# Performance work log

Measured on AMD Instinct MI355X. Metric: run time of the kernel, lower is better.

Reference implementation:

```python
import jax, jax.numpy as jnp
import numpy as np

B, S, D, H = 1, 4096, 1024, 16
HD = D // H

def setup_inputs() -> dict:
    key = jax.random.key(0)
    ks = jax.random.split(key, 6)
    scale = 0.02
    return {
        "x":  jax.random.normal(ks[0], (B, S, D), dtype=jnp.float32),
        "Wq": jax.random.normal(ks[1], (D, D), dtype=jnp.float32) * scale,
        "Wk": jax.random.normal(ks[2], (D, D), dtype=jnp.float32) * scale,
        "Wv": jax.random.normal(ks[3], (D, D), dtype=jnp.float32) * scale,
        "Wo": jax.random.normal(ks[4], (D, D), dtype=jnp.float32) * scale,
        "bo": jnp.zeros((D,), dtype=jnp.float32),
    }

def reference(x, Wq, Wk, Wv, Wo, bo):
    b, s, d = x.shape
    # torch Linear: y = x @ W.T (weights stored [out,in])
    def proj(W):
        return (x @ W.T).reshape(b, s, H, HD).transpose(0, 2, 1, 3)  # [b,h,s,hd]
    q, k, v = proj(Wq), proj(Wk), proj(Wv)
    scores = jnp.einsum('bhqd,bhkd->bhqk', q, k)  # [b,h,s,s]
    causal = jnp.tril(jnp.ones((s, s), dtype=bool))
    scores = jnp.where(causal, scores, -jnp.inf)
    weights = jax.nn.softmax(scores / np.sqrt(HD).astype(np.float32), axis=-1)
    ctx = jnp.einsum('bhqk,bhkd->bhqd', weights, v)
    ctx = ctx.transpose(0, 2, 1, 3).reshape(b, s, d)
    return ctx @ Wo.T + bo
```

## Files before the change

kernel.cpp:

```cpp
#include <hip/hip_runtime.h>
#include <stdint.h>

typedef unsigned short u16;
typedef __attribute__((ext_vector_type(4))) unsigned short u16x4;
typedef __attribute__((ext_vector_type(8))) unsigned short u16x8;
typedef __attribute__((ext_vector_type(8))) __bf16 bf16x8;
typedef __attribute__((ext_vector_type(4))) float f32x4;

#define S_LEN 4096
#define D_DIM 1024
#define NH    16
#define HD    64

__device__ __forceinline__ u16 f2bf(float f) {
  return __builtin_bit_cast(u16, (__bf16)f);
}
__device__ __forceinline__ float bf2f(u16 v) {
  return __builtin_bit_cast(float, (uint32_t)v << 16);
}
__device__ __forceinline__ bf16x8 bc(u16x8 v) { return __builtin_bit_cast(bf16x8, v); }
__device__ __forceinline__ float fexp2(float x) { return __builtin_amdgcn_exp2f(x); }

__device__ __forceinline__ void gload16(const u16* g, u16* l) {
  __builtin_amdgcn_global_load_lds((__attribute__((address_space(1))) void*)g,
                                   (__attribute__((address_space(3))) void*)l, 16, 0, 0);
}

__global__ __launch_bounds__(256) void conv_all_kernel(const float* __restrict__ x,
                                                       const float* __restrict__ Wq,
                                                       const float* __restrict__ Wk,
                                                       const float* __restrict__ Wv,
                                                       const float* __restrict__ Wo,
                                                       u16* __restrict__ Xb, u16* __restrict__ Wqb,
                                                       u16* __restrict__ Wkb, u16* __restrict__ Wvb,
                                                       u16* __restrict__ Wob) {
  int blk = blockIdx.x;
  const float* src;
  u16* dst;
  int i;
  if (blk < 4096) { src = x; dst = Xb; i = blk * 256 + threadIdx.x; }
  else {
    int wi = (blk - 4096) >> 10;
    int lb = (blk - 4096) & 1023;
    src = (wi == 0) ? Wq : (wi == 1) ? Wk : (wi == 2) ? Wv : Wo;
    dst = (wi == 0) ? Wqb : (wi == 1) ? Wkb : (wi == 2) ? Wvb : Wob;
    i = lb * 256 + threadIdx.x;
  }
  f32x4 v = ((const f32x4*)src)[i];
  u16x4 o;
  o[0] = f2bf(v[0]); o[1] = f2bf(v[1]); o[2] = f2bf(v[2]); o[3] = f2bf(v[3]);
  ((u16x4*)dst)[i] = o;
}

__device__ __forceinline__ void gemm_core(const u16* __restrict__ A,
                                          const u16* __restrict__ W,
                                          int m0, int n0, int Kd,
                                          u16* As, u16* Bs, f32x4 acc[4][4]) {
  const int tid  = threadIdx.x;
  const int lane = tid & 63;
  const int wv   = tid >> 6;
  const int wr   = wv >> 1, wc = wv & 1;
  const int b    = lane & 15, quad = lane >> 4;
  const int lrow = lane >> 2;
  const int cg   = ((lane & 3) - (lrow >> 1)) & 3;
  const int goff = ((quad + (b >> 1)) & 3) * 8;

  const u16* ga0 = A + (size_t)(m0 + wv * 16 + lrow) * Kd + cg * 8;
  const u16* ga1 = A + (size_t)(m0 + 64 + wv * 16 + lrow) * Kd + cg * 8;
  const u16* gb0 = W + (size_t)(n0 + wv * 16 + lrow) * Kd + cg * 8;
  const u16* gb1 = W + (size_t)(n0 + 64 + wv * 16 + lrow) * Kd + cg * 8;
  u16* la0 = As + wv * 512;
  u16* la1 = As + 2048 + wv * 512;
  u16* lb0 = Bs + wv * 512;
  u16* lb1 = Bs + 2048 + wv * 512;

  for (int k0 = 0; k0 < Kd; k0 += 32) {
    gload16(ga0 + k0, la0);
    gload16(ga1 + k0, la1);
    gload16(gb0 + k0, lb0);
    gload16(gb1 + k0, lb1);
    __syncthreads();

    u16x8 af[4], bw[4];
#pragma unroll
    for (int i = 0; i < 4; ++i) {
      af[i] = *(const u16x8*)(As + (wr * 64 + i * 16 + b) * 32 + goff);
      bw[i] = *(const u16x8*)(Bs + (wc * 64 + i * 16 + b) * 32 + goff);
    }
#pragma unroll
    for (int i = 0; i < 4; ++i)
#pragma unroll
      for (int j = 0; j < 4; ++j)
        acc[i][j] = __builtin_amdgcn_mfma_f32_16x16x32_bf16(bc(af[i]), bc(bw[j]), acc[i][j], 0, 0, 0);
    __syncthreads();
  }
}

__global__ __launch_bounds__(256) void gemm_qkv_kernel(const u16* __restrict__ X,
                                                       const u16* __restrict__ Wq,
                                                       const u16* __restrict__ Wk,
                                                       const u16* __restrict__ Wv,
                                                       u16* __restrict__ Q,
                                                       u16* __restrict__ K,
                                                       u16* __restrict__ Vt) {
  __shared__ __align__(16) u16 As[128 * 32];
  __shared__ __align__(16) u16 Bs[128 * 32];
  const int z = blockIdx.z;
  const u16* W = (z == 0) ? Wq : (z == 1) ? Wk : Wv;
  const int n0 = blockIdx.x * 128, m0 = blockIdx.y * 128;

  const f32x4 zero4 = {0.f, 0.f, 0.f, 0.f};
  f32x4 acc[4][4];
#pragma unroll
  for (int i = 0; i < 4; ++i)
#pragma unroll
    for (int j = 0; j < 4; ++j) acc[i][j] = zero4;

  gemm_core(X, W, m0, n0, D_DIM, As, Bs, acc);

  const int lane = threadIdx.x & 63;
  const int wv = threadIdx.x >> 6, wr = wv >> 1, wc = wv & 1;
  const int b = lane & 15, quad = lane >> 4;

  if (z < 2) {
    u16* out = (z == 0) ? Q : K;
    const float sc = (z == 0) ? 0.18033688011112042f : 1.0f;
#pragma unroll
    for (int i = 0; i < 4; ++i)
#pragma unroll
      for (int j = 0; j < 4; ++j)
#pragma unroll
        for (int r = 0; r < 4; ++r) {
          int row = m0 + wr * 64 + i * 16 + quad * 4 + r;
          int col = n0 + wc * 64 + j * 16 + b;
          out[(size_t)row * D_DIM + col] = f2bf(acc[i][j][r] * sc);
        }
  } else {
#pragma unroll
    for (int i = 0; i < 4; ++i)
#pragma unroll
      for (int j = 0; j < 4; ++j) {
        int col = n0 + wc * 64 + j * 16 + b;
        int row = m0 + wr * 64 + i * 16 + quad * 4;
        u16x4 vv;
#pragma unroll
        for (int r = 0; r < 4; ++r) vv[r] = f2bf(acc[i][j][r]);
        *(u16x4*)(Vt + (size_t)col * S_LEN + row) = vv;
      }
  }
}

__global__ __launch_bounds__(512) void attn_kernel(const u16* __restrict__ Q,
                                                   const u16* __restrict__ K,
                                                   const u16* __restrict__ Vt,
                                                   u16* __restrict__ Opart,
                                                   float* __restrict__ ml) {
  const int u = (int)gridDim.x - 1 - (int)blockIdx.x;
  const int h = u / 80;
  const int uu = u - h * 80;
  int qt, c;
  if (uu < 8)       { qt = uu;                    c = 0; }
  else if (uu < 24) { qt = 8 + ((uu - 8) >> 1);   c = (uu - 8) & 1; }
  else if (uu < 48) { qt = 16 + (uu - 24) / 3;    c = (uu - 24) % 3; }
  else              { qt = 24 + ((uu - 48) >> 2); c = (uu - 48) & 3; }
  const int t0 = c * 16;
  const int t_end = min(t0 + 16, 2 * qt + 2);
  const int q0 = qt * 128;

  const int tid = threadIdx.x, lane = tid & 63, w = tid >> 6;
  const int quad = lane >> 4, b = lane & 15;
  const int lrow = lane >> 2;
  const int cg   = ((lane & 3) - (lrow >> 1)) & 3;
  const int goff = ((quad + (b >> 1)) & 3) * 8;

  __shared__ __align__(16) u16 Ks[2 * 4096];
  __shared__ __align__(16) u16 Vts[2 * 4096];
  __shared__ __align__(16) u16 Ps[8][16 * 72];

  const int ksg = w & 1, rg = w >> 1;
  const u16* kgb = K + (size_t)(rg * 16 + lrow) * D_DIM + h * HD + ksg * 32 + cg * 8;
  const u16* vgb = Vt + (size_t)(h * HD + rg * 16 + lrow) * S_LEN + ksg * 32 + cg * 8;
  u16* const ldk = Ks + ksg * 2048 + rg * 512;
  u16* const ldv = Vts + ksg * 2048 + rg * 512;

  u16x8 bq[2];
  {
    const size_t qbase = (size_t)(q0 + w * 16 + b) * D_DIM + h * HD + quad * 8;
    bq[0] = *(const u16x8*)(Q + qbase);
    bq[1] = *(const u16x8*)(Q + qbase + 32);
  }

  const f32x4 zero4 = {0.f, 0.f, 0.f, 0.f};
  f32x4 o[4];
#pragma unroll
  for (int jt = 0; jt < 4; ++jt) o[jt] = zero4;
  float m_run = -3.0e38f, l_run = 0.f;

  auto stage = [&](int t, int bsel) {
    gload16(kgb + (size_t)t * 64 * D_DIM, ldk + bsel * 4096);
    gload16(vgb + t * 64, ldv + bsel * 4096);
  };

  u16* PsW = &Ps[w][0];
  const int qg = q0 + w * 16 + b;
  const int qg_wmax = q0 + w * 16 + 15;
  stage(t0, 0);
  int buf = 0;

  for (int t = t0; t < t_end; ++t) {
    __syncthreads();
    if (t + 1 < t_end) stage(t + 1, buf ^ 1);

    if (t * 64 <= qg_wmax) {
      const u16* KB = Ks + buf * 4096;
      const u16* VB = Vts + buf * 4096;

      f32x4 s[4];
#pragma unroll
      for (int jt = 0; jt < 4; ++jt) {
        s[jt] = zero4;
#pragma unroll
        for (int ks = 0; ks < 2; ++ks) {
          u16x8 ak = *(const u16x8*)(KB + ks * 2048 + jt * 512 + b * 32 + goff);
          s[jt] = __builtin_amdgcn_mfma_f32_16x16x32_bf16(bc(ak), bc(bq[ks]), s[jt], 0, 0, 0);
        }
      }

      if (t * 64 + 63 > qg) {
        const int kvb = t * 64 + quad * 4;
#pragma unroll
        for (int jt = 0; jt < 4; ++jt)
#pragma unroll
          for (int r = 0; r < 4; ++r)
            if (kvb + jt * 16 + r > qg) s[jt][r] = -1.0e30f;
      }

      float mx = s[0][0];
#pragma unroll
      for (int jt = 0; jt < 4; ++jt)
#pragma unroll
        for (int r = 0; r < 4; ++r) mx = fmaxf(mx, s[jt][r]);
      mx = fmaxf(mx, __shfl_xor(mx, 16));
      mx = fmaxf(mx, __shfl_xor(mx, 32));

      const float mn = fmaxf(m_run, mx);
      const float alpha = fexp2(m_run - mn);
      m_run = mn;

      float sum = 0.f;
#pragma unroll
      for (int jt = 0; jt < 4; ++jt) {
        u16x4 pk;
#pragma unroll
        for (int r = 0; r < 4; ++r) {
          float p = fexp2(s[jt][r] - mn);
          sum += p;
          pk[r] = f2bf(p);
        }
        *(u16x4*)(PsW + b * 72 + jt * 16 + quad * 4) = pk;
      }
      sum += __shfl_xor(sum, 16);
      sum += __shfl_xor(sum, 32);
      l_run = l_run * alpha + sum;

#pragma unroll
      for (int jt = 0; jt < 4; ++jt) o[jt] *= alpha;

      u16x8 bp[2];
      bp[0] = *(const u16x8*)(PsW + b * 72 + quad * 8);
      bp[1] = *(const u16x8*)(PsW + b * 72 + 32 + quad * 8);
#pragma unroll
      for (int jt = 0; jt < 4; ++jt)
#pragma unroll
        for (int ks = 0; ks < 2; ++ks) {
          u16x8 av = *(const u16x8*)(VB + ks * 2048 + jt * 512 + b * 32 + goff);
          o[jt] = __builtin_amdgcn_mfma_f32_16x16x32_bf16(bc(av), bc(bp[ks]), o[jt], 0, 0, 0);
        }
    }
    buf ^= 1;
  }

  const size_t ob = (size_t)u * 8192 + (size_t)(w * 16 + b) * 64 + quad * 4;
#pragma unroll
  for (int jt = 0; jt < 4; ++jt) {
    u16x4 ov;
#pragma unroll
    for (int r = 0; r < 4; ++r) ov[r] = f2bf(o[jt][r]);
    *(u16x4*)(Opart + ob + jt * 16) = ov;
  }
  if (quad == 0) {
    ml[(size_t)u * 256 + w * 16 + b]       = m_run;
    ml[(size_t)u * 256 + 128 + w * 16 + b] = l_run;
  }
}

__global__ __launch_bounds__(256) void attn_combine_kernel(const u16* __restrict__ Opart,
                                                           const float* __restrict__ ml,
                                                           u16* __restrict__ Ctx) {
  const int hq = blockIdx.x;
  const int h = hq >> 6, qt64 = hq & 63;
  const int qt = qt64 >> 1;
  int base;
  if (qt < 8)       base = qt;
  else if (qt < 16) base = 2 * qt - 8;
  else if (qt < 24) base = 3 * qt - 24;
  else              base = 4 * qt - 48;
  base += h * 80;
  const int nc = 1 + (qt >> 3);

  const int tid = threadIdx.x;
  const int row = tid >> 2;
  const int urow = (qt64 & 1) * 64 + row;
  const int dg  = (tid & 3) * 16;

  float M = -3.0e38f;
  for (int ci = 0; ci < nc; ++ci)
    M = fmaxf(M, ml[(size_t)(base + ci) * 256 + urow]);

  float L = 0.f;
  float acc[16];
#pragma unroll
  for (int i = 0; i < 16; ++i) acc[i] = 0.f;

  for (int ci = 0; ci < nc; ++ci) {
    float mp = ml[(size_t)(base + ci) * 256 + urow];
    float lp = ml[(size_t)(base + ci) * 256 + 128 + urow];
    float wgt = fexp2(mp - M);
    L += lp * wgt;
    const u16* op = Opart + (size_t)(base + ci) * 8192 + (size_t)urow * 64 + dg;
    u16x8 v0 = *(const u16x8*)op;
    u16x8 v1 = *(const u16x8*)(op + 8);
#pragma unroll
    for (int i = 0; i < 8; ++i) acc[i] += bf2f(v0[i]) * wgt;
#pragma unroll
    for (int i = 0; i < 8; ++i) acc[i + 8] += bf2f(v1[i]) * wgt;
  }
  const float inv = 1.f / L;
  u16x8 o0, o1;
#pragma unroll
  for (int i = 0; i < 8; ++i) { o0[i] = f2bf(acc[i] * inv); o1[i] = f2bf(acc[i + 8] * inv); }
  u16* dst = Ctx + (size_t)(qt64 * 64 + row) * D_DIM + h * HD + dg;
  *(u16x8*)dst = o0;
  *(u16x8*)(dst + 8) = o1;
}

__global__ __launch_bounds__(256) void gemm_out_kernel(const u16* __restrict__ Ctx,
                                                       const u16* __restrict__ Wo,
                                                       const float* __restrict__ bo,
                                                       float* __restrict__ out) {
  __shared__ __align__(16) u16 As[128 * 32];
  __shared__ __align__(16) u16 Bs[128 * 32];
  const int n0 = blockIdx.x * 128, m0 = blockIdx.y * 128;

  const f32x4 zero4 = {0.f, 0.f, 0.f, 0.f};
  f32x4 acc[4][4];
#pragma unroll
  for (int i = 0; i < 4; ++i)
#pragma unroll
    for (int j = 0; j < 4; ++j) acc[i][j] = zero4;

  gemm_core(Ctx, Wo, m0, n0, D_DIM, As, Bs, acc);

  const int lane = threadIdx.x & 63;
  const int wv = threadIdx.x >> 6, wr = wv >> 1, wc = wv & 1;
  const int b = lane & 15, quad = lane >> 4;

#pragma unroll
  for (int j = 0; j < 4; ++j) {
    int col = n0 + wc * 64 + j * 16 + b;
    float bias = bo[col];
#pragma unroll
    for (int i = 0; i < 4; ++i)
#pragma unroll
      for (int r = 0; r < 4; ++r) {
        int row = m0 + wr * 64 + i * 16 + quad * 4 + r;
        out[(size_t)row * D_DIM + col] = acc[i][j][r] + bias;
      }
  }
}

extern "C" void kernel_launch(void* const* d_in, const int* in_sizes, int n_in,
                              void* d_out, int out_size, void* d_ws, size_t ws_size,
                              hipStream_t stream) {
  const float* x  = (const float*)d_in[0];
  const float* Wq = (const float*)d_in[1];
  const float* Wk = (const float*)d_in[2];
  const float* Wv = (const float*)d_in[3];
  const float* Wo = (const float*)d_in[4];
  const float* bo = (const float*)d_in[5];
  float* out = (float*)d_out;

  char* ws = (char*)d_ws;
  const size_t MB = 1u << 20;
  u16*   Xb    = (u16*)(ws + 0 * MB);
  u16*   Wqb   = (u16*)(ws + 8 * MB);
  u16*   Wkb   = (u16*)(ws + 10 * MB);
  u16*   Wvb   = (u16*)(ws + 12 * MB);
  u16*   Wob   = (u16*)(ws + 14 * MB);
  u16*   Qb    = (u16*)(ws + 16 * MB);
  u16*   Kb    = (u16*)(ws + 24 * MB);
  u16*   Vtb   = (u16*)(ws + 32 * MB);
  u16*   Cxb   = (u16*)(ws + 40 * MB);
  u16*   Opart = (u16*)(ws + 48 * MB);
  float* mlbuf = (float*)(ws + 68 * MB);

  conv_all_kernel<<<8192, 256, 0, stream>>>(x, Wq, Wk, Wv, Wo, Xb, Wqb, Wkb, Wvb, Wob);

  gemm_qkv_kernel<<<dim3(D_DIM / 128, S_LEN / 128, 3), 256, 0, stream>>>(
      Xb, Wqb, Wkb, Wvb, Qb, Kb, Vtb);

  attn_kernel<<<dim3(1280), 512, 0, stream>>>(Qb, Kb, Vtb, Opart, mlbuf);

  attn_combine_kernel<<<dim3(1024), 256, 0, stream>>>(Opart, mlbuf, Cxb);

  gemm_out_kernel<<<dim3(D_DIM / 128, S_LEN / 128), 256, 0, stream>>>(Cxb, Wob, bo, out);
}
```

Measured before the change: 214.1 us.

## Use 32x32x16 MFMA in attention with 4 waves and double-buffer GEMM tiles

The attention kernel moves from 8 waves issuing 16x16x32 MFMAs to 4 waves issuing 32x32x16 MFMAs. Each wave now handles 32 query rows, and the K/V shared-memory layout uses a new XOR swizzle. Separately, the GEMM core double-buffers its LDS tiles, prefetching the next K-slice before the MFMAs and dropping the second barrier. The aim is fewer LDS reads per FLOP, less softmax shuffle work, and overlap of global loads with compute, at the cost of more registers per wave and lower wave count per block.

```diff
diff --git a/kernel.cpp b/kernel.cpp
--- a/kernel.cpp
+++ b/kernel.cpp
@@ -6,6 +6,7 @@
 typedef __attribute__((ext_vector_type(8))) unsigned short u16x8;
 typedef __attribute__((ext_vector_type(8))) __bf16 bf16x8;
 typedef __attribute__((ext_vector_type(4))) float f32x4;
+typedef __attribute__((ext_vector_type(16))) float f32x16;
 
 #define S_LEN 4096
 #define D_DIM 1024
@@ -74,25 +75,33 @@
   u16* lb0 = Bs + wv * 512;
   u16* lb1 = Bs + 2048 + wv * 512;
 
+  auto stage = [&](int k0, int bsel) {
+    gload16(ga0 + k0, la0 + bsel * 4096);
+    gload16(ga1 + k0, la1 + bsel * 4096);
+    gload16(gb0 + k0, lb0 + bsel * 4096);
+    gload16(gb1 + k0, lb1 + bsel * 4096);
+  };
+
+  stage(0, 0);
+  int buf = 0;
   for (int k0 = 0; k0 < Kd; k0 += 32) {
-    gload16(ga0 + k0, la0);
-    gload16(ga1 + k0, la1);
-    gload16(gb0 + k0, lb0);
-    gload16(gb1 + k0, lb1);
     __syncthreads();
-
+    if (k0 + 32 < Kd) stage(k0 + 32, buf ^ 1);
+
+    const u16* AB = As + buf * 4096;
+    const u16* BB = Bs + buf * 4096;
     u16x8 af[4], bw[4];
 #pragma unroll
     for (int i = 0; i < 4; ++i) {
-      af[i] = *(const u16x8*)(As + (wr * 64 + i * 16 + b) * 32 + goff);
-      bw[i] = *(const u16x8*)(Bs + (wc * 64 + i * 16 + b) * 32 + goff);
+      af[i] = *(const u16x8*)(AB + (wr * 64 + i * 16 + b) * 32 + goff);
+      bw[i] = *(const u16x8*)(BB + (wc * 64 + i * 16 + b) * 32 + goff);
     }
 #pragma unroll
     for (int i = 0; i < 4; ++i)
 #pragma unroll
       for (int j = 0; j < 4; ++j)
         acc[i][j] = __builtin_amdgcn_mfma_f32_16x16x32_bf16(bc(af[i]), bc(bw[j]), acc[i][j], 0, 0, 0);
-    __syncthreads();
+    buf ^= 1;
   }
 }
 
@@ -103,8 +112,8 @@
                                                        u16* __restrict__ Q,
                                                        u16* __restrict__ K,
                                                        u16* __restrict__ Vt) {
-  __shared__ __align__(16) u16 As[128 * 32];
-  __shared__ __align__(16) u16 Bs[128 * 32];
+  __shared__ __align__(16) u16 As[2 * 4096];
+  __shared__ __align__(16) u16 Bs[2 * 4096];
   const int z = blockIdx.z;
   const u16* W = (z == 0) ? Wq : (z == 1) ? Wk : Wv;
   const int n0 = blockIdx.x * 128, m0 = blockIdx.y * 128;
@@ -150,7 +159,7 @@
   }
 }
 
-__global__ __launch_bounds__(512) void attn_kernel(const u16* __restrict__ Q,
+__global__ __launch_bounds__(256) void attn_kernel(const u16* __restrict__ Q,
                                                    const u16* __restrict__ K,
                                                    const u16* __restrict__ Vt,
                                                    u16* __restrict__ Opart,
@@ -168,42 +177,46 @@
   const int q0 = qt * 128;
 
   const int tid = threadIdx.x, lane = tid & 63, w = tid >> 6;
-  const int quad = lane >> 4, b = lane & 15;
-  const int lrow = lane >> 2;
-  const int cg   = ((lane & 3) - (lrow >> 1)) & 3;
-  const int goff = ((quad + (b >> 1)) & 3) * 8;
-
-  __shared__ __align__(16) u16 Ks[2 * 4096];
-  __shared__ __align__(16) u16 Vts[2 * 4096];
-  __shared__ __align__(16) u16 Ps[8][16 * 72];
-
-  const int ksg = w & 1, rg = w >> 1;
-  const u16* kgb = K + (size_t)(rg * 16 + lrow) * D_DIM + h * HD + ksg * 32 + cg * 8;
-  const u16* vgb = Vt + (size_t)(h * HD + rg * 16 + lrow) * S_LEN + ksg * 32 + cg * 8;
-  u16* const ldk = Ks + ksg * 2048 + rg * 512;
-  u16* const ldv = Vts + ksg * 2048 + rg * 512;
-
-  u16x8 bq[2];
+  const int half = lane >> 5;
+  const int l31 = lane & 31;
+
+  __shared__ __align__(16) u16 Ks[2][4096];
+  __shared__ __align__(16) u16 Vts[2][4096];
+  __shared__ __align__(16) u16 Ps[4][32 * 72];
+
+  const int sr    = lane >> 3;
+  const int srow  = w * 16 + sr;
+  const int clog  = ((lane & 7) - sr) & 7;
+  const u16* kgb = K + (size_t)srow * D_DIM + h * HD + clog * 8;
+  const u16* vgb = Vt + (size_t)(h * HD + srow) * S_LEN + clog * 8;
+  u16* const ldk = &Ks[0][0] + w * 16 * 64;
+  u16* const ldv = &Vts[0][0] + w * 16 * 64;
+
+  auto stage = [&](int t, int bsel) {
+    const u16* kg = kgb + (size_t)t * 64 * D_DIM;
+    const u16* vg = vgb + t * 64;
+    gload16(kg, ldk + bsel * 4096);
+    gload16(kg + 8 * D_DIM, ldk + bsel * 4096 + 512);
+    gload16(vg, ldv + bsel * 4096);
+    gload16(vg + 8 * S_LEN, ldv + bsel * 4096 + 512);
+  };
+
+  u16x8 bq[4];
   {
-    const size_t qbase = (size_t)(q0 + w * 16 + b) * D_DIM + h * HD + quad * 8;
-    bq[0] = *(const u16x8*)(Q + qbase);
-    bq[1] = *(const u16x8*)(Q + qbase + 32);
-  }
-
-  const f32x4 zero4 = {0.f, 0.f, 0.f, 0.f};
-  f32x4 o[4];
-#pragma unroll
-  for (int jt = 0; jt < 4; ++jt) o[jt] = zero4;
+    const u16* qp = Q + (size_t)(q0 + w * 32 + l31) * D_DIM + h * HD + half * 8;
+#pragma unroll
+    for (int dt = 0; dt < 4; ++dt) bq[dt] = *(const u16x8*)(qp + dt * 16);
+  }
+
+  const f32x16 zero16 = {0.f,0.f,0.f,0.f,0.f,0.f,0.f,0.f,0.f,0.f,0.f,0.f,0.f,0.f,0.f,0.f};
+  f32x16 ot[2];
+  ot[0] = zero16; ot[1] = zero16;
   float m_run = -3.0e38f, l_run = 0.f;
 
-  auto stage = [&](int t, int bsel) {
-    gload16(kgb + (size_t)t * 64 * D_DIM, ldk + bsel * 4096);
-    gload16(vgb + t * 64, ldv + bsel * 4096);
-  };
-
-  u16* PsW = &Ps[w][0];
-  const int qg = q0 + w * 16 + b;
-  const int qg_wmax = q0 + w * 16 + 15;
+  u16* const PsW = &Ps[w][0];
+  const int qg = q0 + w * 32 + l31;
+  const int qg_wmax = q0 + w * 32 + 31;
+
   stage(t0, 0);
   int buf = 0;
 
@@ -212,35 +225,36 @@
     if (t + 1 < t_end) stage(t + 1, buf ^ 1);
 
     if (t * 64 <= qg_wmax) {
-      const u16* KB = Ks + buf * 4096;
-      const u16* VB = Vts + buf * 4096;
-
-      f32x4 s[4];
-#pragma unroll
-      for (int jt = 0; jt < 4; ++jt) {
-        s[jt] = zero4;
-#pragma unroll
-        for (int ks = 0; ks < 2; ++ks) {
-          u16x8 ak = *(const u16x8*)(KB + ks * 2048 + jt * 512 + b * 32 + goff);
-          s[jt] = __builtin_amdgcn_mfma_f32_16x16x32_bf16(bc(ak), bc(bq[ks]), s[jt], 0, 0, 0);
+      const u16* KB = &Ks[buf][0];
+      const u16* VB = &Vts[buf][0];
+
+      f32x16 s[2];
+      s[0] = zero16; s[1] = zero16;
+#pragma unroll
+      for (int jt = 0; jt < 2; ++jt) {
+        const int row = jt * 32 + l31;
+#pragma unroll
+        for (int dt = 0; dt < 4; ++dt) {
+          u16x8 ak = *(const u16x8*)(KB + row * 64 + (((dt * 2 + half) + row) & 7) * 8);
+          s[jt] = __builtin_amdgcn_mfma_f32_32x32x16_bf16(bc(ak), bc(bq[dt]), s[jt], 0, 0, 0);
         }
       }
 
       if (t * 64 + 63 > qg) {
-        const int kvb = t * 64 + quad * 4;
-#pragma unroll
-        for (int jt = 0; jt < 4; ++jt)
-#pragma unroll
-          for (int r = 0; r < 4; ++r)
-            if (kvb + jt * 16 + r > qg) s[jt][r] = -1.0e30f;
+#pragma unroll
+        for (int jt = 0; jt < 2; ++jt) {
+          const int kvb = t * 64 + jt * 32 + 4 * half;
+#pragma unroll
+          for (int e = 0; e < 16; ++e)
+            if (kvb + (e & 3) + 8 * (e >> 2) > qg) s[jt][e] = -1.0e30f;
+        }
       }
 
-      float mx = s[0][0];
-#pragma unroll
-      for (int jt = 0; jt < 4; ++jt)
-#pragma unroll
-        for (int r = 0; r < 4; ++r) mx = fmaxf(mx, s[jt][r]);
-      mx = fmaxf(mx, __shfl_xor(mx, 16));
+      float mx = -3.0e38f;
+#pragma unroll
+      for (int jt = 0; jt < 2; ++jt)
+#pragma unroll
+        for (int e = 0; e < 16; ++e) mx = fmaxf(mx, s[jt][e]);
       mx = fmaxf(mx, __shfl_xor(mx, 32));
 
       const float mn = fmaxf(m_run, mx);
@@ -249,48 +263,51 @@
 
       float sum = 0.f;
 #pragma unroll
-      for (int jt = 0; jt < 4; ++jt) {
-        u16x4 pk;
-#pragma unroll
-        for (int r = 0; r < 4; ++r) {
-          float p = fexp2(s[jt][r] - mn);
-          sum += p;
-          pk[r] = f2bf(p);
+      for (int jt = 0; jt < 2; ++jt)
+#pragma unroll
+        for (int g = 0; g < 4; ++g) {
+          u16x4 pk;
+#pragma unroll
+          for (int r = 0; r < 4; ++r) {
+            float p = fexp2(s[jt][4 * g + r] - mn);
+            sum += p;
+            pk[r] = f2bf(p);
+          }
+          *(u16x4*)(PsW + l31 * 72 + jt * 32 + 4 * half + 8 * g) = pk;
         }
-        *(u16x4*)(PsW + b * 72 + jt * 16 + quad * 4) = pk;
-      }
-      sum += __shfl_xor(sum, 16);
       sum += __shfl_xor(sum, 32);
       l_run = l_run * alpha + sum;
 
-#pragma unroll
-      for (int jt = 0; jt < 4; ++jt) o[jt] *= alpha;
-
-      u16x8 bp[2];
-      bp[0] = *(const u16x8*)(PsW + b * 72 + quad * 8);
-      bp[1] = *(const u16x8*)(PsW + b * 72 + 32 + quad * 8);
-#pragma unroll
-      for (int jt = 0; jt < 4; ++jt)
-#pragma unroll
-        for (int ks = 0; ks < 2; ++ks) {
-          u16x8 av = *(const u16x8*)(VB + ks * 2048 + jt * 512 + b * 32 + goff);
-          o[jt] = __builtin_amdgcn_mfma_f32_16x16x32_bf16(bc(av), bc(bp[ks]), o[jt], 0, 0, 0);
+      ot[0] *= alpha;
+      ot[1] *= alpha;
+
+#pragma unroll
+      for (int kt = 0; kt < 4; ++kt) {
+        u16x8 bp = *(const u16x8*)(PsW + l31 * 72 + kt * 16 + half * 8);
+#pragma unroll
+        for (int dt2 = 0; dt2 < 2; ++dt2) {
+          const int row = dt2 * 32 + l31;
+          u16x8 av = *(const u16x8*)(VB + row * 64 + (((kt * 2 + half) + row) & 7) * 8);
+          ot[dt2] = __builtin_amdgcn_mfma_f32_32x32x16_bf16(bc(av), bc(bp), ot[dt2], 0, 0, 0);
         }
+      }
     }
     buf ^= 1;
   }
 
-  const size_t ob = (size_t)u * 8192 + (size_t)(w * 16 + b) * 64 + quad * 4;
-#pragma unroll
-  for (int jt = 0; jt < 4; ++jt) {
-    u16x4 ov;
-#pragma unroll
-    for (int r = 0; r < 4; ++r) ov[r] = f2bf(o[jt][r]);
-    *(u16x4*)(Opart + ob + jt * 16) = ov;
-  }
-  if (quad == 0) {
-    ml[(size_t)u * 256 + w * 16 + b]       = m_run;
-    ml[(size_t)u * 256 + 128 + w * 16 + b] = l_run;
+  const size_t ob = (size_t)u * 8192 + (size_t)(w * 32 + l31) * 64 + 4 * half;
+#pragma unroll
+  for (int dt2 = 0; dt2 < 2; ++dt2)
+#pragma unroll
+    for (int g = 0; g < 4; ++g) {
+      u16x4 ov;
+#pragma unroll
+      for (int r = 0; r < 4; ++r) ov[r] = f2bf(ot[dt2][4 * g + r]);
+      *(u16x4*)(Opart + ob + dt2 * 32 + 8 * g) = ov;
+    }
+  if (lane < 32) {
+    ml[(size_t)u * 256 + w * 32 + lane]       = m_run;
+    ml[(size_t)u * 256 + 128 + w * 32 + lane] = l_run;
   }
 }
 
@@ -348,8 +365,8 @@
                                                        const u16* __restrict__ Wo,
                                                        const float* __restrict__ bo,
                                                        float* __restrict__ out) {
-  __shared__ __align__(16) u16 As[128 * 32];
-  __shared__ __align__(16) u16 Bs[128 * 32];
+  __shared__ __align__(16) u16 As[2 * 4096];
+  __shared__ __align__(16) u16 Bs[2 * 4096];
   const int n0 = blockIdx.x * 128, m0 = blockIdx.y * 128;
 
   const f32x4 zero4 = {0.f, 0.f, 0.f, 0.f};
@@ -409,7 +426,7 @@
   gemm_qkv_kernel<<<dim3(D_DIM / 128, S_LEN / 128, 3), 256, 0, stream>>>(
       Xb, Wqb, Wkb, Wvb, Qb, Kb, Vtb);
 
-  attn_kernel<<<dim3(1280), 512, 0, stream>>>(Qb, Kb, Vtb, Opart, mlbuf);
+  attn_kernel<<<dim3(1280), 256, 0, stream>>>(Qb, Kb, Vtb, Opart, mlbuf);
 
   attn_combine_kernel<<<dim3(1024), 256, 0, stream>>>(Opart, mlbuf, Cxb);
 
```

Measured after the change: 216.7 us. About the same (+1.2%).
